# Performance work log

Hardware: AMD Instinct MI355X
Metric: run time of the kernel (lower is better)

The kernel has to match this reference:

```python
import jax, jax.numpy as jnp
import numpy as np

H = 512        # hidden_dim
V = 50257      # num_classes == vocabulary_size
L = 2          # stacked LSTM layers
B = 64         # batch (and n_facts)
T = 64         # n_words per sequence


def _run_layer(x_proj, W_hh):
    """One LSTM layer. x_proj: (B, T, 4H) precomputed input projection (+biases).
    Gate order matches torch: i, f, g, o. Initial h, c are zeros (reset_hidden_state)."""
    Bq = x_proj.shape[0]
    Hq = W_hh.shape[1]

    def step(carry, x_t):
        h, c = carry
        gates = x_t + h @ W_hh.T                      # (B, 4H)
        i, f, g, o = jnp.split(gates, 4, axis=-1)
        i = jax.nn.sigmoid(i)
        f = jax.nn.sigmoid(f)
        g = jnp.tanh(g)
        o = jax.nn.sigmoid(o)
        c = f * c + i * g
        h = o * jnp.tanh(c)
        return (h, c), h

    init = (jnp.zeros((Bq, Hq), x_proj.dtype), jnp.zeros((Bq, Hq), x_proj.dtype))
    _, hs = jax.lax.scan(step, init, x_proj.transpose(1, 0, 2))  # scan over T
    return hs.transpose(1, 0, 2)                       # (B, T, H)


def _lstm_stack(x_idx, params):
    """params: list of L tuples (W_ih, W_hh, b_ih, b_hh).
    Layer 0: one_hot(x) @ W_ih.T == gather of W_ih.T rows (same math, no VxBT one-hot)."""
    W_ih0, W_hh0, b_ih0, b_hh0 = params[0]
    x_proj = W_ih0.T[x_idx] + b_ih0 + b_hh0            # (B, T, 4H) via row gather
    out = _run_layer(x_proj, W_hh0)
    for (W_ih, W_hh, b_ih, b_hh) in params[1:]:
        x_proj = jnp.einsum('bth,gh->btg', out, W_ih) + b_ih + b_hh
        out = _run_layer(x_proj, W_hh)
    return out


def setup_inputs() -> dict:
    key = jax.random.key(0)
    ks = jax.random.split(key, 20)
    s = 1.0 / np.sqrt(H)  # torch LSTM init scale
    inp = {}
    inp['x_q'] = jax.random.randint(ks[0], (B, T), 0, V, dtype=jnp.int64)
    inp['x_f'] = jax.random.randint(ks[1], (B, T), 0, V, dtype=jnp.int64)
    i = 2
    for br in ('q', 'f'):
        for l in range(L):
            in_dim = V if l == 0 else H
            inp[f'Wih_{br}{l}'] = jax.random.uniform(ks[i], (4 * H, in_dim), jnp.float32, -s, s); i += 1
            inp[f'Whh_{br}{l}'] = jax.random.uniform(ks[i], (4 * H, H), jnp.float32, -s, s); i += 1
            inp[f'bih_{br}{l}'] = jax.random.uniform(ks[i], (4 * H,), jnp.float32, -s, s); i += 1
            inp[f'bhh_{br}{l}'] = jax.random.uniform(ks[i], (4 * H,), jnp.float32, -s, s); i += 1
    return inp


def reference(x_q, x_f,
              Wih_q0, Whh_q0, bih_q0, bhh_q0,
              Wih_q1, Whh_q1, bih_q1, bhh_q1,
              Wih_f0, Whh_f0, bih_f0, bhh_f0,
              Wih_f1, Whh_f1, bih_f1, bhh_f1):
    params_q = [(Wih_q0, Whh_q0, bih_q0, bhh_q0), (Wih_q1, Whh_q1, bih_q1, bhh_q1)]
    params_f = [(Wih_f0, Whh_f0, bih_f0, bhh_f0), (Wih_f1, Whh_f1, bih_f1, bhh_f1)]
    out_q = _lstm_stack(x_q, params_q)   # process_query
    out_f = _lstm_stack(x_f, params_f)   # process_facts
    return jnp.stack([out_q, out_f])     # (2, B, T, H)
```

## Files before the change

kernel.cpp:

```cpp
#include <hip/hip_runtime.h>
#include <cstdint>
#include <cstddef>

#define HD 512
#define BB 64
#define TT 64
#define VV 50257
#define GG 2048
#define NBLK 128
#define NTHR 256
#define PS 21
#define GCW 1024
#define GR 8
#define VH 25136
#define SLOTSTRIDE 16

typedef __attribute__((ext_vector_type(8))) short bf16x8;
typedef __attribute__((ext_vector_type(4))) float f32x4;

__device__ __forceinline__ float bf2f(unsigned short u) {
  union { unsigned int i; float f; } v; v.i = ((unsigned int)u) << 16; return v.f;
}
__device__ __forceinline__ unsigned short f2bf(float f) {
  union { float f; unsigned int i; } v; v.f = f;
  unsigned int r = (v.i + 0x7fffu + ((v.i >> 16) & 1u)) >> 16;
  return (unsigned short)r;
}
__device__ __forceinline__ float sigf(float x) { return 1.0f / (1.0f + __expf(-x)); }

__device__ __forceinline__ bf16x8 ldh16(const unsigned short* p) {
  union { unsigned long long q[2]; bf16x8 v; } u;
  const unsigned long long* p64 = (const unsigned long long*)p;
  u.q[0] = __hip_atomic_load(p64,     __ATOMIC_RELAXED, __HIP_MEMORY_SCOPE_AGENT);
  u.q[1] = __hip_atomic_load(p64 + 1, __ATOMIC_RELAXED, __HIP_MEMORY_SCOPE_AGENT);
  return u.v;
}

__global__ void lstm_detect(const unsigned int* whh, const unsigned int* xq, int* flags) {
  __shared__ int csmall, oddnz;
  if (threadIdx.x == 0) { csmall = 0; oddnz = 0; }
  __syncthreads();
  {
    unsigned int w = whh[threadIdx.x];
    union { unsigned int i; float f; } lo; lo.i = w << 16;
    float a = fabsf(lo.f);
    if (a <= 0.0444f) atomicAdd(&csmall, 1);
  }
  if (threadIdx.x < 64) {
    if (xq[2 * threadIdx.x + 1] != 0) atomicAdd(&oddnz, 1);
  }
  __syncthreads();
  if (threadIdx.x == 0) {
    flags[0] = (csmall >= 240) ? 1 : 0;
    flags[1] = (oddnz == 0) ? 1 : 0;
  }
}

struct PrepParams {
  const void* src[18];
  const int* flags;
  unsigned int* bar;
  int* xidx;
  float* bsum0;
  float* bsum1;
  unsigned short* W0;
  unsigned short* W1;
  unsigned short* h0;
  unsigned short* h1;
};

__global__ void lstm_prep(PrepParams p) {
  const int F = p.flags[0];
  const int X = p.flags[1];
  const size_t NW0 = (size_t)2 * GG * HD;
  const size_t NW1 = (size_t)2 * GG * 1024;
  const size_t NBS = (size_t)2 * 2 * GG;
  const size_t NXI = (size_t)2 * BB * TT;
  const size_t NHZ = 262144;
  const size_t NBZ = 2048;
  const size_t TOT = NW0 + NW1 + NBS + NXI + NHZ + NBZ;
  for (size_t g = (size_t)blockIdx.x * blockDim.x + threadIdx.x; g < TOT;
       g += (size_t)gridDim.x * blockDim.x) {
    size_t e = g;
    if (e < NW0) {
      size_t br = e / ((size_t)GG * HD), r = e % ((size_t)GG * HD);
      const void* s = p.src[br ? 11 : 3];
      p.W0[e] = F ? ((const unsigned short*)s)[r] : f2bf(((const float*)s)[r]);
      continue;
    }
    e -= NW0;
    if (e < NW1) {
      size_t br = e / ((size_t)GG * 1024), r = e % ((size_t)GG * 1024);
      size_t col = r >> 10, k = r & 1023;
      const void* s = (k < 512) ? p.src[br ? 14 : 6] : p.src[br ? 15 : 7];
      size_t so = col * HD + (k & 511);
      p.W1[e] = F ? ((const unsigned short*)s)[so] : f2bf(((const float*)s)[so]);
      continue;
    }
    e -= NW1;
    if (e < NBS) {
      size_t br = e / (2 * GG), r = e % (2 * GG);
      size_t layer = r / GG, gg = r % GG;
      const void* s1 = p.src[(br ? 12 : 4) + (layer ? 4 : 0)];
      const void* s2 = p.src[(br ? 13 : 5) + (layer ? 4 : 0)];
      float v1 = F ? bf2f(((const unsigned short*)s1)[gg]) : ((const float*)s1)[gg];
      float v2 = F ? bf2f(((const unsigned short*)s2)[gg]) : ((const float*)s2)[gg];
      (layer ? p.bsum1 : p.bsum0)[br * GG + gg] = v1 + v2;
      continue;
    }
    e -= NBS;
    if (e < NXI) {
      size_t br = e / (BB * TT), r = e % (BB * TT);
      const void* s = p.src[br ? 1 : 0];
      p.xidx[e] = X ? ((const int*)s)[2 * r] : ((const int*)s)[r];
      continue;
    }
    e -= NXI;
    if (e < NHZ) {
      const size_t half = 131072;
      if (e < half) p.h0[e] = 0; else p.h1[e - half] = 0;
      continue;
    }
    e -= NHZ;
    p.bar[e] = 0;
  }
}

struct GatherParams {
  const void* wih0[2];
  const int* xidx;
  void* xp;
  const int* flags;
  int xp32;
};

__launch_bounds__(256, 4)
__global__ void lstm_gather(GatherParams gp) {
  __shared__ float lds[GR][GCW];
  const int tid = threadIdx.x;
  const int branch = blockIdx.x >> 9;
  const int rem = blockIdx.x & 511;
  const int gc = rem >> 1;
  const int half = rem & 1;
  const int g0 = gc * GR;
  const int cbase = half * VH;
  const int cend = (half ? VV : VH);
  const int F = gp.flags[0];
  const int XP = gp.xp32;
  const int t  = tid & 63;
  const int bq = tid >> 6;

  int tok[16];
  const int* xid = gp.xidx + branch * (BB * TT);
#pragma unroll
  for (int i = 0; i < 16; ++i) tok[i] = xid[(bq * 16 + i) * TT + t];

  float* xpf = (float*)gp.xp;
  unsigned short* xpb = (unsigned short*)gp.xp;

  for (int c0 = cbase; c0 < cend; c0 += GCW) {
    const int cs = (cend - c0 < GCW) ? (cend - c0) : GCW;
    if (F) {
      const unsigned short* w = (const unsigned short*)gp.wih0[branch];
#pragma unroll
      for (int r = 0; r < GR; ++r) {
        const unsigned short* row = w + (size_t)(g0 + r) * VV + c0;
        for (int c = tid; c < cs; c += 256) lds[r][c] = bf2f(row[c]);
      }
    } else {
      const float* w = (const float*)gp.wih0[branch];
#pragma unroll
      for (int r = 0; r < GR; ++r) {
        const float* row = w + (size_t)(g0 + r) * VV + c0;
        const int m = (int)(((uintptr_t)row >> 2) & 3);
        int lead = (4 - m) & 3; if (lead > cs) lead = cs;
        if (tid < lead) lds[r][tid] = row[tid];
        const int nv = (cs - lead) >> 2;
        const f32x4* rv = (const f32x4*)(row + lead);
        for (int v = tid; v < nv; v += 256) {
          f32x4 x = rv[v];
          const int d = lead + v * 4;
          lds[r][d] = x[0]; lds[r][d + 1] = x[1]; lds[r][d + 2] = x[2]; lds[r][d + 3] = x[3];
        }
        for (int off2 = lead + nv * 4 + tid; off2 < cs; off2 += 256) lds[r][off2] = row[off2];
      }
    }
    __syncthreads();
#pragma unroll
    for (int i = 0; i < 16; ++i) {
      const unsigned int d = (unsigned int)(tok[i] - c0);
      if (d < (unsigned int)cs) {
        const int b = bq * 16 + i;
        const size_t base = (((size_t)branch * TT + t) * BB + b) * GG + g0;
        if (XP) {
          f32x4 x0 = { lds[0][d], lds[1][d], lds[2][d], lds[3][d] };
          f32x4 x1 = { lds[4][d], lds[5][d], lds[6][d], lds[7][d] };
          *(f32x4*)(xpf + base) = x0;
          *(f32x4*)(xpf + base + 4) = x1;
        } else {
#pragma unroll
          for (int r = 0; r < GR; ++r) xpb[base + r] = f2bf(lds[r][d]);
        }
      }
    }
    __syncthreads();
  }
}

__device__ __forceinline__ void gbar_slots(unsigned int* slots, int myslot,
                                           unsigned int target) {
  __syncthreads();
  if (threadIdx.x < 64) {
    if (threadIdx.x == 0) {
      asm volatile("" ::: "memory");
      __hip_atomic_fetch_add(&slots[myslot * SLOTSTRIDE], 1u,
                             __ATOMIC_RELAXED, __HIP_MEMORY_SCOPE_AGENT);
    }
    const int lane = threadIdx.x;
    bool done;
    do {
      unsigned int v = target;
      if (lane < 32)
        v = __hip_atomic_load(&slots[lane * SLOTSTRIDE],
                              __ATOMIC_RELAXED, __HIP_MEMORY_SCOPE_AGENT);
      done = __all(v >= target);
      if (!done) __builtin_amdgcn_s_sleep(1);
    } while (!done);
    asm volatile("" ::: "memory");
  }
  __syncthreads();
}

struct LstmParams {
  const void* xp;
  const float* bsum0;
  const float* bsum1;
  const unsigned short* W0;
  const unsigned short* W1;
  unsigned short* h0;
  unsigned short* h1;
  unsigned int* bar;
  const int* flags;
  int xp32;
  void* out;
};

__launch_bounds__(NTHR, 1)
__global__ void lstm_main(LstmParams p) {
  __shared__ float P0[4][32][PS];
  __shared__ float P1[4][32][PS];
  __shared__ __attribute__((aligned(16))) unsigned short h0s[32 * 512];
  __shared__ __attribute__((aligned(16))) unsigned short h1s[32 * 512];

  const int tid  = threadIdx.x;
  const int l15  = tid & 15;
  const int lk   = (tid & 63) >> 4;
  const int wid  = tid >> 6;

  const int bid  = blockIdx.x;
  const int xcd  = bid & 7;
  const int rest = bid >> 3;
  const int brr  = (xcd >= 4) ? 1 : 0;
  const int u    = (xcd & 3) + rest * 4;
  const int btile = u & 1;
  const int jblk  = u >> 1;
  const int jcol  = jblk * 16 + l15;
  const int F = p.flags[0];
  const int XP = p.xp32;

  const unsigned short* W0 = p.W0 + (size_t)brr * GG * HD;
  const unsigned short* W1 = p.W1 + (size_t)brr * GG * 1024;
  unsigned short* h0b = p.h0 + (size_t)brr * 2 * BB * HD;
  unsigned short* h1b = p.h1 + (size_t)brr * 2 * BB * HD;
  const float* xpf = (const float*)p.xp;
  const unsigned short* xpb = (const unsigned short*)p.xp;
  unsigned int* slots = p.bar + (brr * 2 + btile) * 32 * SLOTSTRIDE;

  bf16x8 bw0[16], bw1[32];
  {
    const unsigned short* w0r = W0 + (size_t)(wid * HD + jcol) * HD;
    const unsigned short* w1r = W1 + (size_t)(wid * HD + jcol) * 1024;
#pragma unroll
    for (int kc = 0; kc < 16; ++kc)
      bw0[kc] = *(const bf16x8*)(w0r + kc * 32 + lk * 8);
#pragma unroll
    for (int kc = 0; kc < 32; ++kc)
      bw1[kc] = *(const bf16x8*)(w1r + kc * 32 + lk * 8);
  }

  const int rls = tid >> 3;
  const int seg = tid & 7;
  const int growl = btile * 32 + rls;

  const bool upd = (tid < 128);
  const int rl   = tid >> 2;
  const int uq4  = (tid & 3) * 4;
  const int ucol = jblk * 16 + uq4;
  const int ub   = btile * 32 + rl;

  float bs0q[16], bs1q[16];
  if (upd) {
#pragma unroll
    for (int q = 0; q < 4; ++q)
#pragma unroll
      for (int j = 0; j < 4; ++j) {
        bs0q[q * 4 + j] = p.bsum0[brr * GG + q * HD + ucol + j];
        bs1q[q * 4 + j] = p.bsum1[brr * GG + q * HD + ucol + j];
      }
  }

  float c0[4] = {0.f, 0.f, 0.f, 0.f}, c1[4] = {0.f, 0.f, 0.f, 0.f};
  float xgc[16], xgn[16];
  unsigned int dummy = 0;

  auto xoff = [&](int t, int q) -> size_t {
    return (((size_t)brr * TT + t) * BB + ub) * GG + (size_t)q * HD + ucol;
  };
  if (upd) {
#pragma unroll
    for (int q = 0; q < 4; ++q) {
      if (XP) {
        f32x4 v = *(const f32x4*)(xpf + xoff(0, q));
#pragma unroll
        for (int j = 0; j < 4; ++j) xgc[q * 4 + j] = v[j];
      } else {
#pragma unroll
        for (int j = 0; j < 4; ++j) xgc[q * 4 + j] = bf2f(xpb[xoff(0, q) + j]);
      }
    }
  }

  auto frag0 = [&](int rloc, int e0) -> bf16x8 {
    const int be = (e0 * 2) ^ ((rloc & 7) << 4);
    return *(const bf16x8*)&h0s[rloc * 512 + (be >> 1)];
  };
  auto frag1 = [&](int rloc, int e0) -> bf16x8 {
    const int be = (e0 * 2) ^ ((rloc & 7) << 4);
    return *(const bf16x8*)&h1s[rloc * 512 + (be >> 1)];
  };

  for (int s = 0; s <= TT; ++s) {
    const unsigned short* h0r = h0b + (size_t)((s + 1) & 1) * BB * HD;
    const unsigned short* h1p = h1b + (size_t)(s & 1) * BB * HD;
    const bool do0 = (s < TT), do1 = (s >= 1);

    bf16x8 sv0[8], sv1[8];
    {
      const unsigned short* s0 = h0r + (size_t)growl * HD;
      const unsigned short* s1 = h1p + (size_t)growl * HD;
#pragma unroll
      for (int c = 0; c < 8; ++c) {
        sv0[c] = ldh16(s0 + c * 64 + seg * 8);
        sv1[c] = ldh16(s1 + c * 64 + seg * 8);
      }
#pragma unroll
      for (int c = 0; c < 8; ++c) {
        const int be = ((c * 8 + seg) * 16) ^ ((rls & 7) << 4);
        *(bf16x8*)&h0s[rls * 512 + (be >> 1)] = sv0[c];
      }
    }

    if (upd) {
      int tn = s + 1; if (tn > TT - 1) tn = TT - 1;
#pragma unroll
      for (int q = 0; q < 4; ++q) {
        if (XP) {
          f32x4 v = *(const f32x4*)(xpf + xoff(tn, q));
#pragma unroll
          for (int j = 0; j < 4; ++j) xgn[q * 4 + j] = v[j];
        } else {
#pragma unroll
          for (int j = 0; j < 4; ++j) xgn[q * 4 + j] = bf2f(xpb[xoff(tn, q) + j]);
        }
      }
    }
    __syncthreads();

    if (do0) {
      f32x4 acc0[2];
#pragma unroll
      for (int bt = 0; bt < 2; ++bt) acc0[bt] = (f32x4){0.f, 0.f, 0.f, 0.f};
#pragma unroll
      for (int kc = 0; kc < 16; ++kc) {
        const int k0 = kc * 32 + lk * 8;
#pragma unroll
        for (int bt = 0; bt < 2; ++bt) {
          bf16x8 av = frag0(bt * 16 + l15, k0);
          acc0[bt] = __builtin_amdgcn_mfma_f32_16x16x32_bf16(av, bw0[kc], acc0[bt], 0, 0, 0);
        }
      }
#pragma unroll
      for (int bt = 0; bt < 2; ++bt)
#pragma unroll
        for (int i = 0; i < 4; ++i)
          P0[wid][bt * 16 + lk * 4 + i][l15] = acc0[bt][i];
    }

    {
#pragma unroll
      for (int c = 0; c < 8; ++c) {
        const int be = ((c * 8 + seg) * 16) ^ ((rls & 7) << 4);
        *(bf16x8*)&h1s[rls * 512 + (be >> 1)] = sv1[c];
      }
    }
    __syncthreads();

    if (do1) {
      f32x4 acc1[2];
#pragma unroll
      for (int bt = 0; bt < 2; ++bt) acc1[bt] = (f32x4){0.f, 0.f, 0.f, 0.f};
#pragma unroll
      for (int kc = 0; kc < 32; ++kc) {
        const int k0 = kc * 32 + lk * 8;
#pragma unroll
        for (int bt = 0; bt < 2; ++bt) {
          bf16x8 av = (kc < 16) ? frag0(bt * 16 + l15, k0)
                                : frag1(bt * 16 + l15, k0 - 512);
          acc1[bt] = __builtin_amdgcn_mfma_f32_16x16x32_bf16(av, bw1[kc], acc1[bt], 0, 0, 0);
        }
      }
#pragma unroll
      for (int bt = 0; bt < 2; ++bt)
#pragma unroll
        for (int i = 0; i < 4; ++i)
          P1[wid][bt * 16 + lk * 4 + i][l15] = acc1[bt][i];
    }
    __syncthreads();

    if (do0 && upd) {
      unsigned short* h0w = h0b + (size_t)(s & 1) * BB * HD;
      unsigned long long pk = 0ull;
#pragma unroll
      for (int j = 0; j < 4; ++j) {
        float gi = sigf(P0[0][rl][uq4 + j] + bs0q[0 + j] + xgc[0 + j]);
        float gf = sigf(P0[1][rl][uq4 + j] + bs0q[4 + j] + xgc[4 + j]);
        float gc = tanhf(P0[2][rl][uq4 + j] + bs0q[8 + j] + xgc[8 + j]);
        float go = sigf(P0[3][rl][uq4 + j] + bs0q[12 + j] + xgc[12 + j]);
        c0[j] = gf * c0[j] + gi * gc;
        float hv = go * tanhf(c0[j]);
        pk |= (unsigned long long)f2bf(hv) << (16 * j);
      }
      unsigned long long* dst =
          (unsigned long long*)(h0w + (size_t)ub * HD + ucol);
      unsigned long long old =
          __hip_atomic_exchange(dst, pk, __ATOMIC_RELAXED, __HIP_MEMORY_SCOPE_AGENT);
      dummy ^= (unsigned int)(old ^ (old >> 32));
    }
    if (do1 && upd) {
      unsigned short* h1w = h1b + (size_t)((s - 1) & 1) * BB * HD;
      const int tl = s - 1;
      unsigned long long pk = 0ull;
      float hv4[4];
#pragma unroll
      for (int j = 0; j < 4; ++j) {
        float gi = sigf(P1[0][rl][uq4 + j] + bs1q[0 + j]);
        float gf = sigf(P1[1][rl][uq4 + j] + bs1q[4 + j]);
        float gc = tanhf(P1[2][rl][uq4 + j] + bs1q[8 + j]);
        float go = sigf(P1[3][rl][uq4 + j] + bs1q[12 + j]);
        c1[j] = gf * c1[j] + gi * gc;
        hv4[j] = go * tanhf(c1[j]);
        pk |= (unsigned long long)f2bf(hv4[j]) << (16 * j);
      }
      unsigned long long* dst =
          (unsigned long long*)(h1w + (size_t)ub * HD + ucol);
      unsigned long long old =
          __hip_atomic_exchange(dst, pk, __ATOMIC_RELAXED, __HIP_MEMORY_SCOPE_AGENT);
      dummy ^= (unsigned int)(old ^ (old >> 32));
      const size_t oo = (((size_t)brr * BB + ub) * TT + tl) * HD + ucol;
      if (F) {
        *(unsigned long long*)((unsigned short*)p.out + oo) = pk;
      } else {
        f32x4 v = { hv4[0], hv4[1], hv4[2], hv4[3] };
        *(f32x4*)((float*)p.out + oo) = v;
      }
    }

    if (upd) {
#pragma unroll
      for (int i2 = 0; i2 < 16; ++i2) xgc[i2] = xgn[i2];
    }

    if (s < TT) gbar_slots(slots, jblk, (unsigned int)(s + 1));
  }

  if (dummy == 0x9E3779B9u) p.bar[2047] = dummy;
}

extern "C" void kernel_launch(void* const* d_in, const int* in_sizes, int n_in,
                              void* d_out, int out_size, void* d_ws, size_t ws_size,
                              hipStream_t stream) {
  if (n_in < 18) return;
  char* ws = (char*)d_ws;
  size_t off = 0;
  auto alloc = [&](size_t bytes) -> void* {
    off = (off + 255) & ~(size_t)255;
    void* r = ws + off;
    off += bytes;
    return r;
  };
  int* flags           = (int*)alloc(256);
  unsigned int* bar    = (unsigned int*)alloc(8192);
  int* xidx            = (int*)alloc((size_t)2 * BB * TT * 4);
  float* bsum0         = (float*)alloc((size_t)2 * GG * 4);
  float* bsum1         = (float*)alloc((size_t)2 * GG * 4);
  unsigned short* W0   = (unsigned short*)alloc((size_t)2 * GG * HD * 2);
  unsigned short* W1   = (unsigned short*)alloc((size_t)2 * GG * 1024 * 2);
  unsigned short* h0   = (unsigned short*)alloc((size_t)2 * 2 * BB * HD * 2);
  unsigned short* h1   = (unsigned short*)alloc((size_t)2 * 2 * BB * HD * 2);

  const size_t xp_f32_bytes = (size_t)2 * TT * BB * GG * 4;
  const size_t xp_b16_bytes = (size_t)2 * TT * BB * GG * 2;
  int xp32 = (off + 256 + xp_f32_bytes <= ws_size) ? 1 : 0;
  void* xp = alloc(xp32 ? xp_f32_bytes : xp_b16_bytes);
  (void)in_sizes; (void)out_size;

  lstm_detect<<<dim3(1), dim3(256), 0, stream>>>(
      (const unsigned int*)d_in[3], (const unsigned int*)d_in[0], flags);

  PrepParams pp;
  for (int i = 0; i < 18; ++i) pp.src[i] = d_in[i];
  pp.flags = flags; pp.bar = bar; pp.xidx = xidx;
  pp.bsum0 = bsum0; pp.bsum1 = bsum1;
  pp.W0 = W0; pp.W1 = W1; pp.h0 = h0; pp.h1 = h1;
  lstm_prep<<<dim3(1024), dim3(256), 0, stream>>>(pp);

  GatherParams gp;
  gp.wih0[0] = d_in[2]; gp.wih0[1] = d_in[10];
  gp.xidx = xidx; gp.xp = xp; gp.flags = flags; gp.xp32 = xp32;
  lstm_gather<<<dim3(1024), dim3(256), 0, stream>>>(gp);

  LstmParams lp;
  lp.xp = xp; lp.bsum0 = bsum0; lp.bsum1 = bsum1;
  lp.W0 = W0; lp.W1 = W1; lp.h0 = h0; lp.h1 = h1;
  lp.bar = bar; lp.flags = flags; lp.xp32 = xp32; lp.out = d_out;
  lstm_main<<<dim3(NBLK), dim3(NTHR), 0, stream>>>(lp);
}
```

Before: 942.3 us.

## Load recurrent weights directly in main kernel, prefetch gather chunks, drop a barrier

Removes the prep-stage conversion of W_hh/W_ih1 into packed bf16 workspace copies. The main kernel now reads the original weights and converts them to bf16 in registers when it loads them once at startup. The gather kernel becomes software-pipelined: the next column chunk is held in registers while the current chunk is scattered from LDS. The h1 staging store is merged into the h0 store, which removes one __syncthreads per timestep. This trades extra register pressure and uncoalesced fp32 weight reads at startup for less global traffic and less per-step synchronisation.

After: 820.9 us. 12.9% less time.

```diff
diff --git a/kernel.cpp b/kernel.cpp
--- a/kernel.cpp
+++ b/kernel.cpp
@@ -63,8 +63,6 @@
   int* xidx;
   float* bsum0;
   float* bsum1;
-  unsigned short* W0;
-  unsigned short* W1;
   unsigned short* h0;
   unsigned short* h1;
 };
@@ -72,32 +70,14 @@
 __global__ void lstm_prep(PrepParams p) {
   const int F = p.flags[0];
   const int X = p.flags[1];
-  const size_t NW0 = (size_t)2 * GG * HD;
-  const size_t NW1 = (size_t)2 * GG * 1024;
   const size_t NBS = (size_t)2 * 2 * GG;
   const size_t NXI = (size_t)2 * BB * TT;
   const size_t NHZ = 262144;
   const size_t NBZ = 2048;
-  const size_t TOT = NW0 + NW1 + NBS + NXI + NHZ + NBZ;
+  const size_t TOT = NBS + NXI + NHZ + NBZ;
   for (size_t g = (size_t)blockIdx.x * blockDim.x + threadIdx.x; g < TOT;
        g += (size_t)gridDim.x * blockDim.x) {
     size_t e = g;
-    if (e < NW0) {
-      size_t br = e / ((size_t)GG * HD), r = e % ((size_t)GG * HD);
-      const void* s = p.src[br ? 11 : 3];
-      p.W0[e] = F ? ((const unsigned short*)s)[r] : f2bf(((const float*)s)[r]);
-      continue;
-    }
-    e -= NW0;
-    if (e < NW1) {
-      size_t br = e / ((size_t)GG * 1024), r = e % ((size_t)GG * 1024);
-      size_t col = r >> 10, k = r & 1023;
-      const void* s = (k < 512) ? p.src[br ? 14 : 6] : p.src[br ? 15 : 7];
-      size_t so = col * HD + (k & 511);
-      p.W1[e] = F ? ((const unsigned short*)s)[so] : f2bf(((const float*)s)[so]);
-      continue;
-    }
-    e -= NW1;
     if (e < NBS) {
       size_t br = e / (2 * GG), r = e % (2 * GG);
       size_t layer = r / GG, gg = r % GG;
@@ -158,34 +138,44 @@
   float* xpf = (float*)gp.xp;
   unsigned short* xpb = (unsigned short*)gp.xp;
 
-  for (int c0 = cbase; c0 < cend; c0 += GCW) {
-    const int cs = (cend - c0 < GCW) ? (cend - c0) : GCW;
+  float rg[GR][4];
+  auto issue = [&](int c0, int cs) {
     if (F) {
       const unsigned short* w = (const unsigned short*)gp.wih0[branch];
 #pragma unroll
-      for (int r = 0; r < GR; ++r) {
-        const unsigned short* row = w + (size_t)(g0 + r) * VV + c0;
-        for (int c = tid; c < cs; c += 256) lds[r][c] = bf2f(row[c]);
-      }
+      for (int r = 0; r < GR; ++r)
+#pragma unroll
+        for (int j = 0; j < 4; ++j) {
+          const int c = tid + j * 256;
+          rg[r][j] = (c < cs) ? bf2f(w[(size_t)(g0 + r) * VV + c0 + c]) : 0.f;
+        }
     } else {
       const float* w = (const float*)gp.wih0[branch];
 #pragma unroll
-      for (int r = 0; r < GR; ++r) {
-        const float* row = w + (size_t)(g0 + r) * VV + c0;
-        const int m = (int)(((uintptr_t)row >> 2) & 3);
-        int lead = (4 - m) & 3; if (lead > cs) lead = cs;
-        if (tid < lead) lds[r][tid] = row[tid];
-        const int nv = (cs - lead) >> 2;
-        const f32x4* rv = (const f32x4*)(row + lead);
-        for (int v = tid; v < nv; v += 256) {
-          f32x4 x = rv[v];
-          const int d = lead + v * 4;
-          lds[r][d] = x[0]; lds[r][d + 1] = x[1]; lds[r][d + 2] = x[2]; lds[r][d + 3] = x[3];
+      for (int r = 0; r < GR; ++r)
+#pragma unroll
+        for (int j = 0; j < 4; ++j) {
+          const int c = tid + j * 256;
+          rg[r][j] = (c < cs) ? w[(size_t)(g0 + r) * VV + c0 + c] : 0.f;
         }
-        for (int off2 = lead + nv * 4 + tid; off2 < cs; off2 += 256) lds[r][off2] = row[off2];
-      }
-    }
+    }
+  };
+
+  int c0 = cbase;
+  int cs = (cend - c0 < GCW) ? (cend - c0) : GCW;
+  issue(c0, cs);
+  for (;;) {
+#pragma unroll
+    for (int r = 0; r < GR; ++r)
+#pragma unroll
+      for (int j = 0; j < 4; ++j)
+        lds[r][tid + j * 256] = rg[r][j];
     __syncthreads();
+
+    const int c1 = c0 + GCW;
+    const int cs1 = (c1 < cend) ? ((cend - c1 < GCW) ? (cend - c1) : GCW) : 0;
+    if (cs1 > 0) issue(c1, cs1);
+
 #pragma unroll
     for (int i = 0; i < 16; ++i) {
       const unsigned int d = (unsigned int)(tok[i] - c0);
@@ -204,6 +194,8 @@
       }
     }
     __syncthreads();
+    if (cs1 == 0) break;
+    c0 = c1; cs = cs1;
   }
 }
 
@@ -235,8 +227,9 @@
   const void* xp;
   const float* bsum0;
   const float* bsum1;
-  const unsigned short* W0;
-  const unsigned short* W1;
+  const void* whh0[2];
+  const void* wih1[2];
+  const void* whh1[2];
   unsigned short* h0;
   unsigned short* h1;
   unsigned int* bar;
@@ -268,24 +261,36 @@
   const int F = p.flags[0];
   const int XP = p.xp32;
 
-  const unsigned short* W0 = p.W0 + (size_t)brr * GG * HD;
-  const unsigned short* W1 = p.W1 + (size_t)brr * GG * 1024;
   unsigned short* h0b = p.h0 + (size_t)brr * 2 * BB * HD;
   unsigned short* h1b = p.h1 + (size_t)brr * 2 * BB * HD;
   const float* xpf = (const float*)p.xp;
   const unsigned short* xpb = (const unsigned short*)p.xp;
   unsigned int* slots = p.bar + (brr * 2 + btile) * 32 * SLOTSTRIDE;
 
+  auto ldw8 = [&](const void* srcp, size_t eoff) -> bf16x8 {
+    if (F) return *(const bf16x8*)((const unsigned short*)srcp + eoff);
+    const float* f = (const float*)srcp + eoff;
+    f32x4 a = *(const f32x4*)f;
+    f32x4 b = *(const f32x4*)(f + 4);
+    bf16x8 r;
+    r[0] = (short)f2bf(a[0]); r[1] = (short)f2bf(a[1]);
+    r[2] = (short)f2bf(a[2]); r[3] = (short)f2bf(a[3]);
+    r[4] = (short)f2bf(b[0]); r[5] = (short)f2bf(b[1]);
+    r[6] = (short)f2bf(b[2]); r[7] = (short)f2bf(b[3]);
+    return r;
+  };
   bf16x8 bw0[16], bw1[32];
   {
-    const unsigned short* w0r = W0 + (size_t)(wid * HD + jcol) * HD;
-    const unsigned short* w1r = W1 + (size_t)(wid * HD + jcol) * 1024;
+    const size_t grow = (size_t)(wid * HD + jcol);
 #pragma unroll
     for (int kc = 0; kc < 16; ++kc)
-      bw0[kc] = *(const bf16x8*)(w0r + kc * 32 + lk * 8);
-#pragma unroll
-    for (int kc = 0; kc < 32; ++kc)
-      bw1[kc] = *(const bf16x8*)(w1r + kc * 32 + lk * 8);
+      bw0[kc] = ldw8(p.whh0[brr], grow * 512 + kc * 32 + lk * 8);
+#pragma unroll
+    for (int kc = 0; kc < 16; ++kc)
+      bw1[kc] = ldw8(p.wih1[brr], grow * 512 + kc * 32 + lk * 8);
+#pragma unroll
+    for (int kc = 16; kc < 32; ++kc)
+      bw1[kc] = ldw8(p.whh1[brr], grow * 512 + (kc - 16) * 32 + lk * 8);
   }
 
   const int rls = tid >> 3;
@@ -344,10 +349,10 @@
     const unsigned short* h1p = h1b + (size_t)(s & 1) * BB * HD;
     const bool do0 = (s < TT), do1 = (s >= 1);
 
-    bf16x8 sv0[8], sv1[8];
     {
       const unsigned short* s0 = h0r + (size_t)growl * HD;
       const unsigned short* s1 = h1p + (size_t)growl * HD;
+      bf16x8 sv0[8], sv1[8];
 #pragma unroll
       for (int c = 0; c < 8; ++c) {
         sv0[c] = ldh16(s0 + c * 64 + seg * 8);
@@ -357,6 +362,7 @@
       for (int c = 0; c < 8; ++c) {
         const int be = ((c * 8 + seg) * 16) ^ ((rls & 7) << 4);
         *(bf16x8*)&h0s[rls * 512 + (be >> 1)] = sv0[c];
+        *(bf16x8*)&h1s[rls * 512 + (be >> 1)] = sv1[c];
       }
     }
 
@@ -395,16 +401,6 @@
         for (int i = 0; i < 4; ++i)
           P0[wid][bt * 16 + lk * 4 + i][l15] = acc0[bt][i];
     }
-
-    {
-#pragma unroll
-      for (int c = 0; c < 8; ++c) {
-        const int be = ((c * 8 + seg) * 16) ^ ((rls & 7) << 4);
-        *(bf16x8*)&h1s[rls * 512 + (be >> 1)] = sv1[c];
-      }
-    }
-    __syncthreads();
-
     if (do1) {
       f32x4 acc1[2];
 #pragma unroll
@@ -503,8 +499,6 @@
   int* xidx            = (int*)alloc((size_t)2 * BB * TT * 4);
   float* bsum0         = (float*)alloc((size_t)2 * GG * 4);
   float* bsum1         = (float*)alloc((size_t)2 * GG * 4);
-  unsigned short* W0   = (unsigned short*)alloc((size_t)2 * GG * HD * 2);
-  unsigned short* W1   = (unsigned short*)alloc((size_t)2 * GG * 1024 * 2);
   unsigned short* h0   = (unsigned short*)alloc((size_t)2 * 2 * BB * HD * 2);
   unsigned short* h1   = (unsigned short*)alloc((size_t)2 * 2 * BB * HD * 2);
 
@@ -521,8 +515,8 @@
   for (int i = 0; i < 18; ++i) pp.src[i] = d_in[i];
   pp.flags = flags; pp.bar = bar; pp.xidx = xidx;
   pp.bsum0 = bsum0; pp.bsum1 = bsum1;
-  pp.W0 = W0; pp.W1 = W1; pp.h0 = h0; pp.h1 = h1;
-  lstm_prep<<<dim3(1024), dim3(256), 0, stream>>>(pp);
+  pp.h0 = h0; pp.h1 = h1;
+  lstm_prep<<<dim3(256), dim3(256), 0, stream>>>(pp);
 
   GatherParams gp;
   gp.wih0[0] = d_in[2]; gp.wih0[1] = d_in[10];
@@ -531,7 +525,10 @@
 
   LstmParams lp;
   lp.xp = xp; lp.bsum0 = bsum0; lp.bsum1 = bsum1;
-  lp.W0 = W0; lp.W1 = W1; lp.h0 = h0; lp.h1 = h1;
+  lp.whh0[0] = d_in[3];  lp.whh0[1] = d_in[11];
+  lp.wih1[0] = d_in[6];  lp.wih1[1] = d_in[14];
+  lp.whh1[0] = d_in[7];  lp.whh1[1] = d_in[15];
+  lp.h0 = h0; lp.h1 = h1;
   lp.bar = bar; lp.flags = flags; lp.xp32 = xp32; lp.out = d_out;
   lstm_main<<<dim3(NBLK), dim3(NTHR), 0, stream>>>(lp);
 }
```
